# Kernel tuning notes

Measured on AMD Instinct MI355X. Metric: run time of the kernel, lower is better.

Reference implementation:

```python
import jax, jax.numpy as jnp
import numpy as np
import math

B, T, D, H = 4, 1024, 1024, 16
HD = D // H  # 64
ROPE_BASE = 10000.0


def _apply_rope(q, k):
    # q, k: [B, H, T, HD]; interleaved even/odd rotation as in RotaryEmbedding
    t_len = q.shape[2]
    half = q.shape[-1] // 2
    inv_freq = 1.0 / (ROPE_BASE ** (jnp.arange(half, dtype=jnp.float32) / half))
    freqs = jnp.arange(t_len, dtype=jnp.float32)[:, None] * inv_freq  # [T, half]
    cos = jnp.cos(freqs)
    sin = jnp.sin(freqs)

    def rot(u):
        u1 = u[..., ::2]   # even lanes
        u2 = u[..., 1::2]  # odd lanes
        e = u1 * cos - u2 * sin
        o = u2 * cos + u1 * sin
        return jnp.stack([e, o], axis=-1).reshape(u.shape)

    return rot(q), rot(k)


def _split_heads(x):
    b, t, d = x.shape
    return x.reshape(b, t, H, HD).transpose(0, 2, 1, 3)  # [B,H,T,HD]


def _mha(x, Wq, bq, Wk, bk, Wv, bv, Wo, bo, mask):
    q = _split_heads(jnp.einsum('btd,ed->bte', x, Wq) + bq)
    k = _split_heads(jnp.einsum('btd,ed->bte', x, Wk) + bk)
    v = _split_heads(jnp.einsum('btd,ed->bte', x, Wv) + bv)
    q, k = _apply_rope(q, k)
    scores = jnp.einsum('bhtd,bhsd->bhts', q.astype(jnp.float32),
                        k.astype(jnp.float32)) / math.sqrt(HD)
    scores = jnp.where(mask, scores, -jnp.inf)
    attn = jax.nn.softmax(scores, axis=-1).astype(v.dtype)
    ctx = jnp.einsum('bhts,bhsd->bhtd', attn.astype(jnp.float32),
                     v.astype(jnp.float32)).astype(v.dtype)
    ctx = ctx.transpose(0, 2, 1, 3).reshape(x.shape[0], x.shape[1], D)
    z = jnp.einsum('btd,ed->bte', ctx, Wo) + bo
    return z


def setup_inputs() -> dict:
    key = jax.random.key(0)
    ks = jax.random.split(key, 9)
    s = 0.02
    inp = {
        'x':  jax.random.normal(ks[0], (B, T, D), jnp.float32),
        'Wq': jax.random.normal(ks[1], (D, D), jnp.float32) * s,
        'bq': jax.random.normal(ks[2], (D,), jnp.float32) * s,
        'Wk': jax.random.normal(ks[3], (D, D), jnp.float32) * s,
        'bk': jax.random.normal(ks[4], (D,), jnp.float32) * s,
        'Wv': jax.random.normal(ks[5], (D, D), jnp.float32) * s,
        'bv': jax.random.normal(ks[6], (D,), jnp.float32) * s,
        'Wo': jax.random.normal(ks[7], (D, D), jnp.float32) * s,
        'bo': jax.random.normal(ks[8], (D,), jnp.float32) * s,
        'mask': jnp.tril(jnp.ones((T, T), dtype=bool))[None, None],  # causal
    }
    return inp


def reference(x, Wq, bq, Wk, bk, Wv, bv, Wo, bo, mask):
    return _mha(x, Wq, bq, Wk, bk, Wv, bv, Wo, bo, mask)
```

## Files before the change

kernel.cpp:

```cpp
#include <hip/hip_runtime.h>


#define T_SEQ 1024
#define NH    16
#define HDIM  64
#define DM    1024
#define MTOK  4096

typedef __attribute__((ext_vector_type(8))) short short8;
typedef __attribute__((ext_vector_type(4))) float f32x4;
typedef unsigned short u16;

__device__ __forceinline__ u16 f2bf(float f) {
  unsigned int u = __builtin_bit_cast(unsigned int, f);
  u += 0x7fffu + ((u >> 16) & 1u);
  return (u16)(u >> 16);
}

__device__ __forceinline__ void gll16(const void* g, void* l) {
  __builtin_amdgcn_global_load_lds(
      (const __attribute__((address_space(1))) unsigned int*)(unsigned long long)(g),
      (__attribute__((address_space(3))) unsigned int*)(unsigned int)(unsigned long long)(l),
      16, 0, 0);
}

__global__ void prep_kernel(const float* __restrict__ x,
                            const float* __restrict__ Wq, const float* __restrict__ Wk,
                            const float* __restrict__ Wv, const float* __restrict__ Wo,
                            u16* __restrict__ xb, u16* __restrict__ wall,
                            float* __restrict__ ctab, float* __restrict__ stab) {
  const int bid = blockIdx.x, tid = threadIdx.x;
  if (bid < 8192) {
    const float* src;
    u16* dst;
    int i;
    if (bid < 4096) {
      src = x; dst = xb; i = bid * 256 + tid;
    } else {
      const int w = (bid - 4096) >> 10;
      src = w == 0 ? Wq : w == 1 ? Wk : w == 2 ? Wv : Wo;
      dst = wall + (size_t)w * (DM * DM);
      i = ((bid - 4096) & 1023) * 256 + tid;
    }
    float4 f = ((const float4*)src)[i];
    unsigned long long pk = (unsigned long long)f2bf(f.x)
                          | ((unsigned long long)f2bf(f.y) << 16)
                          | ((unsigned long long)f2bf(f.z) << 32)
                          | ((unsigned long long)f2bf(f.w) << 48);
    ((unsigned long long*)dst)[i] = pk;
  } else {
    const int idx = (bid - 8192) * 256 + tid;
    const int t = idx >> 5, i = idx & 31;
    float inv = powf(10000.f, -(float)i * (1.0f / 32.0f));
    float f = (float)t * inv;
    ctab[idx] = cosf(f);
    stab[idx] = sinf(f);
  }
}

template<int BM, int BN, int AI, int BI, int MI, int NJ>
__device__ __forceinline__ void gemm_pipe2(
    const u16* __restrict__ A, const u16* __restrict__ Bw,
    int m0, int n0, u16* As, u16* Bs, f32x4 acc[MI][NJ]) {
  const int tid = threadIdx.x, lane = tid & 63, wave = tid >> 6;
  const int wr = wave >> 1, wc = wave & 1;
  const int srcswz = ((lane & 7) ^ (lane >> 3)) * 8;
  const int NT = DM / 64;

#define STAGE2(t, b)                                                         \
  do {                                                                       \
    _Pragma("unroll") for (int i = 0; i < AI; ++i) {                         \
      const int q = (wave * AI + i) * 64 + lane;                             \
      gll16(&A[(size_t)(m0 + (q >> 3)) * DM + (t) * 64 + srcswz],            \
            &As[(b) * BM * 64 + q * 8]);                                     \
    }                                                                        \
    _Pragma("unroll") for (int i = 0; i < BI; ++i) {                         \
      const int q = (wave * BI + i) * 64 + lane;                             \
      gll16(&Bw[(size_t)(n0 + (q >> 3)) * DM + (t) * 64 + srcswz],           \
            &Bs[(b) * BN * 64 + q * 8]);                                     \
    }                                                                        \
  } while (0)

  STAGE2(0, 0);
  __syncthreads();
  int buf = 0;
  const int arow0 = wr * (BM / 2) + (lane & 15);
  const int brow0 = wc * (BN / 2) + (lane & 15);
  const int c0 = (((lane >> 4)) ^ (lane & 7)) * 8;
  const int c1 = ((4 + (lane >> 4)) ^ (lane & 7)) * 8;
  for (int t = 0; t < NT; ++t) {
    if (t + 1 < NT) STAGE2(t + 1, buf ^ 1);
    short8 af[MI][2], bf[NJ][2];
#pragma unroll
    for (int i = 0; i < MI; ++i) {
      const int r = buf * BM * 64 + (arow0 + i * 16) * 64;
      af[i][0] = *(const short8*)&As[r + c0];
      af[i][1] = *(const short8*)&As[r + c1];
    }
#pragma unroll
    for (int j = 0; j < NJ; ++j) {
      const int r = buf * BN * 64 + (brow0 + j * 16) * 64;
      bf[j][0] = *(const short8*)&Bs[r + c0];
      bf[j][1] = *(const short8*)&Bs[r + c1];
    }
#pragma unroll
    for (int i = 0; i < MI; ++i)
#pragma unroll
      for (int j = 0; j < NJ; ++j) {
        acc[i][j] = __builtin_amdgcn_mfma_f32_16x16x32_bf16(af[i][0], bf[j][0], acc[i][j], 0, 0, 0);
        acc[i][j] = __builtin_amdgcn_mfma_f32_16x16x32_bf16(af[i][1], bf[j][1], acc[i][j], 0, 0, 0);
      }
    __syncthreads();
    buf ^= 1;
  }
#undef STAGE2
}

__global__ __launch_bounds__(256, 2) void qkv_kernel(
    const u16* __restrict__ xb, const u16* __restrict__ wqkv,
    const float* __restrict__ bq, const float* __restrict__ bk, const float* __restrict__ bv,
    const float* __restrict__ ctab, const float* __restrict__ stab,
    u16* __restrict__ qbuf, u16* __restrict__ kbuf, u16* __restrict__ vt) {
  __shared__ __align__(16) u16 As[2 * 128 * 64];
  __shared__ __align__(16) u16 Bs[2 * 192 * 64];
  const int lin = blockIdx.x;
  const int m0 = (lin & 31) * 128;
  const int n0 = (lin >> 5) * 192;
  f32x4 acc[4][6];
#pragma unroll
  for (int i = 0; i < 4; ++i)
#pragma unroll
    for (int j = 0; j < 6; ++j)
#pragma unroll
      for (int r = 0; r < 4; ++r) acc[i][j][r] = 0.f;
  gemm_pipe2<128, 192, 4, 6, 4, 6>(xb, wqkv, m0, n0, As, Bs, acc);

  const int lane = threadIdx.x & 63, wave = threadIdx.x >> 6;
  const int wr = wave >> 1, wc = wave & 1;
#pragma unroll
  for (int i = 0; i < 4; ++i) {
#pragma unroll
    for (int j = 0; j < 6; ++j) {
      const int e = n0 + wc * 96 + j * 16 + (lane & 15);
      const int mode = e >> 10;
      const float* bias = mode == 0 ? bq : (mode == 1 ? bk : bv);
      const float bval = bias[e & 1023];
      const int h = (e >> 6) & 15, hd = e & 63;
#pragma unroll
      for (int r = 0; r < 4; ++r) {
        const int m = m0 + wr * 64 + i * 16 + ((lane >> 4) * 4) + r;
        const int b = m >> 10, t = m & 1023;
        float v = acc[i][j][r] + bval;
        if (mode < 2) {
          float p = __shfl_xor(v, 1);
          const int fi = hd >> 1;
          const float cc = ctab[t * 32 + fi], ss = stab[t * 32 + fi];
          v = (hd & 1) ? (v * cc + p * ss) : (v * cc - p * ss);
          u16* dst = mode == 0 ? qbuf : kbuf;
          dst[(((size_t)(b * NH + h) * T_SEQ + t) << 6) + hd] = f2bf(v);
        } else {
          vt[(((size_t)(b * NH + h) * HDIM + hd) << 10) + t] = f2bf(v);
        }
      }
    }
  }
}

__global__ __launch_bounds__(256) void attn_kernel(
    const u16* __restrict__ qbuf, const u16* __restrict__ kbuf,
    const u16* __restrict__ vtb, u16* __restrict__ ctx) {
  __shared__ __align__(16) u16 Ks[2][64 * 64];
  __shared__ __align__(16) u16 Vs[2][64 * 64];
  __shared__ __align__(16) u16 Psm[4][16 * 64];
  const int bh = blockIdx.x;
  const int b = bh >> 4, h = bh & 15;
  const int tid = threadIdx.x, lane = tid & 63, wave = tid >> 6;
  const u16* Qp = qbuf + (size_t)bh * T_SEQ * HDIM;
  const u16* Kp = kbuf + (size_t)bh * T_SEQ * HDIM;
  const u16* Vp = vtb + (size_t)bh * HDIM * T_SEQ;
  u16* Pw = &Psm[wave][0];
  const float SC = 0.18033688f;

  const int srow = tid >> 3;
  const int schx = ((tid & 7) ^ (srow & 7)) * 8;
  const int lx = lane & 7;

  short8 onesf;
#pragma unroll
  for (int i = 0; i < 8; ++i) onesf[i] = (short)0x3F80;

#define STG(kvt, bb)                                                            \
  do {                                                                          \
    _Pragma("unroll") for (int c = 0; c < 2; ++c) {                             \
      const int rr = c * 32 + srow;                                             \
      gll16(&Kp[(kvt) * 4096 + rr * 64 + schx], &Ks[bb][c * 2048 + tid * 8]);   \
      gll16(&Vp[(size_t)rr * T_SEQ + (kvt) * 64 + schx], &Vs[bb][c * 2048 + tid * 8]); \
    }                                                                           \
  } while (0)

  for (int phase = 0; phase < 2; ++phase) {
    const int qt = phase ? (15 - (int)blockIdx.y) : (int)blockIdx.y;
    const int q0 = qt * 64;
    const int nkv = qt + 1;
    const int qrow = q0 + wave * 16 + (lane & 15);
    const short8 qf0 = *(const short8*)&Qp[qrow * 64 + ((lane >> 4) * 8)];
    const short8 qf1 = *(const short8*)&Qp[qrow * 64 + 32 + ((lane >> 4) * 8)];

    f32x4 acc_o[4], accl;
    float m_r[4];
#pragma unroll
    for (int i = 0; i < 4; ++i) {
#pragma unroll
      for (int r = 0; r < 4; ++r) acc_o[i][r] = 0.f;
      accl[i] = 0.f;
      m_r[i] = -__builtin_inff();
    }

    __syncthreads();
    STG(0, 0);
    int cur = 0;

    for (int kvt = 0; kvt < nkv; ++kvt) {
      __syncthreads();
      if (kvt + 1 < nkv) STG(kvt + 1, cur ^ 1);

      f32x4 sacc[4];
#pragma unroll
      for (int cb = 0; cb < 4; ++cb) {
#pragma unroll
        for (int r = 0; r < 4; ++r) sacc[cb][r] = 0.f;
        const int krow = cb * 16 + (lane & 15);
        const short8 kf0 = *(const short8*)&Ks[cur][krow * 64 + (((lane >> 4) ^ lx) * 8)];
        const short8 kf1 = *(const short8*)&Ks[cur][krow * 64 + (((4 + (lane >> 4)) ^ lx) * 8)];
        sacc[cb] = __builtin_amdgcn_mfma_f32_16x16x32_bf16(qf0, kf0, sacc[cb], 0, 0, 0);
        sacc[cb] = __builtin_amdgcn_mfma_f32_16x16x32_bf16(qf1, kf1, sacc[cb], 0, 0, 0);
      }
      if (kvt == qt) {
        const int trow_base = q0 + wave * 16 + ((lane >> 4) * 4);
#pragma unroll
        for (int cb = 0; cb < 4; ++cb) {
          const int scol = kvt * 64 + cb * 16 + (lane & 15);
#pragma unroll
          for (int r = 0; r < 4; ++r)
            sacc[cb][r] = (scol > trow_base + r) ? -__builtin_inff() : sacc[cb][r] * SC;
        }
      } else {
#pragma unroll
        for (int cb = 0; cb < 4; ++cb)
#pragma unroll
          for (int r = 0; r < 4; ++r) sacc[cb][r] *= SC;
      }
      float mt[4];
#pragma unroll
      for (int r = 0; r < 4; ++r)
        mt[r] = fmaxf(fmaxf(sacc[0][r], sacc[1][r]), fmaxf(sacc[2][r], sacc[3][r]));
#pragma unroll
      for (int off = 1; off < 16; off <<= 1)
#pragma unroll
        for (int r = 0; r < 4; ++r) mt[r] = fmaxf(mt[r], __shfl_xor(mt[r], off));
      float sf[4];
#pragma unroll
      for (int r = 0; r < 4; ++r) {
        const float mn = fmaxf(m_r[r], mt[r]);
        sf[r] = exp2f(m_r[r] - mn);
        m_r[r] = mn;
      }
#pragma unroll
      for (int cb = 0; cb < 4; ++cb)
#pragma unroll
        for (int r = 0; r < 4; ++r) sacc[cb][r] = exp2f(sacc[cb][r] - m_r[r]);
#pragma unroll
      for (int r = 0; r < 4; ++r) accl[r] *= sf[r];
#pragma unroll
      for (int hb = 0; hb < 4; ++hb)
#pragma unroll
        for (int r = 0; r < 4; ++r) acc_o[hb][r] *= sf[r];

#pragma unroll
      for (int cb = 0; cb < 4; ++cb)
#pragma unroll
        for (int r = 0; r < 4; ++r) {
          const int prow = (lane >> 4) * 4 + r;
          Pw[prow * 64 + ((cb * 16 + (lane & 15)) ^ ((prow & 7) << 3))] = f2bf(sacc[cb][r]);
        }

      const int prr = lane & 15;
#pragma unroll
      for (int kc = 0; kc < 2; ++kc) {
        const short8 pf = *(const short8*)&Pw[prr * 64 + (((kc * 4 + (lane >> 4)) ^ lx) * 8)];
        accl = __builtin_amdgcn_mfma_f32_16x16x32_bf16(pf, onesf, accl, 0, 0, 0);
#pragma unroll
        for (int hb = 0; hb < 4; ++hb) {
          const int vrow = hb * 16 + (lane & 15);
          const short8 vf = *(const short8*)&Vs[cur][vrow * 64 + (((kc * 4 + (lane >> 4)) ^ lx) * 8)];
          acc_o[hb] = __builtin_amdgcn_mfma_f32_16x16x32_bf16(pf, vf, acc_o[hb], 0, 0, 0);
        }
      }
      cur ^= 1;
    }

#pragma unroll
    for (int hb = 0; hb < 4; ++hb) {
      const int hd = hb * 16 + (lane & 15);
#pragma unroll
      for (int r = 0; r < 4; ++r) {
        const int t = q0 + wave * 16 + ((lane >> 4) * 4) + r;
        const float v = acc_o[hb][r] / accl[r];
        ctx[((size_t)(b * T_SEQ + t) * NH + h) * HDIM + hd] = f2bf(v);
      }
    }
  }
#undef STG
}

__global__ __launch_bounds__(256, 2) void oproj_kernel(
    const u16* __restrict__ ctx, const u16* __restrict__ Wob,
    const float* __restrict__ bo, float* __restrict__ out) {
  __shared__ __align__(16) u16 As[2 * 64 * 64];
  __shared__ __align__(16) u16 Bs[2 * 128 * 64];
  const int lin = blockIdx.x;
  const int m0 = (lin & 63) * 64;
  const int n0 = (lin >> 6) * 128;
  f32x4 acc[2][4];
#pragma unroll
  for (int i = 0; i < 2; ++i)
#pragma unroll
    for (int j = 0; j < 4; ++j)
#pragma unroll
      for (int r = 0; r < 4; ++r) acc[i][j][r] = 0.f;
  gemm_pipe2<64, 128, 2, 4, 2, 4>(ctx, Wob, m0, n0, As, Bs, acc);
  const int lane = threadIdx.x & 63, wave = threadIdx.x >> 6;
  const int wr = wave >> 1, wc = wave & 1;
#pragma unroll
  for (int i = 0; i < 2; ++i)
#pragma unroll
    for (int j = 0; j < 4; ++j) {
      const int e = n0 + wc * 64 + j * 16 + (lane & 15);
      const float bval = bo[e];
#pragma unroll
      for (int r = 0; r < 4; ++r) {
        const int m = m0 + wr * 32 + i * 16 + ((lane >> 4) * 4) + r;
        out[(size_t)m * DM + e] = acc[i][j][r] + bval;
      }
    }
}

extern "C" void kernel_launch(void* const* d_in, const int* in_sizes, int n_in,
                              void* d_out, int out_size, void* d_ws, size_t ws_size,
                              hipStream_t stream) {
  const float* x  = (const float*)d_in[0];
  const float* Wq = (const float*)d_in[1];
  const float* bq = (const float*)d_in[2];
  const float* Wk = (const float*)d_in[3];
  const float* bk = (const float*)d_in[4];
  const float* Wv = (const float*)d_in[5];
  const float* bv = (const float*)d_in[6];
  const float* Wo = (const float*)d_in[7];
  const float* bo = (const float*)d_in[8];

  char* w = (char*)d_ws;
  u16* xb   = (u16*)(w);
  u16* wall = (u16*)(w + (8ull << 20));
  u16* wob  = (u16*)(w + (14ull << 20));
  u16* qb   = (u16*)(w + (16ull << 20));
  u16* kb   = (u16*)(w + (24ull << 20));
  u16* vtb  = (u16*)(w + (32ull << 20));
  u16* ctxb = (u16*)(w + (40ull << 20));
  float* ctab = (float*)(w + (48ull << 20));
  float* stab = ctab + T_SEQ * 32;

  prep_kernel<<<dim3(8192 + 128), 256, 0, stream>>>(x, Wq, Wk, Wv, Wo, xb, wall, ctab, stab);
  qkv_kernel<<<dim3(512), 256, 0, stream>>>(
      xb, wall, bq, bk, bv, ctab, stab, qb, kb, vtb);
  attn_kernel<<<dim3(64, 8), 256, 0, stream>>>(qb, kb, vtb, ctxb);
  oproj_kernel<<<dim3(512), 256, 0, stream>>>(ctxb, wob, bo, (float*)d_out);
}
```

Measured before the change: 110.6 us.

## Double attention KV tile to 128 and remap QKV GEMM grid to 2D

The attention kernel now processes 128 keys per iteration instead of 64, using dynamic shared memory (80 KB) for double-buffered K/V tiles and wider per-wave P buffers. This halves the loop trip count, cutting per-iteration barriers and softmax reductions, but wastes more masked work on the diagonal tile and may lower occupancy because of the larger LDS footprint. The QKV GEMM launch also moves from a linear grid to a 2D grid, which changes the block ordering and therefore L2 reuse of weight versus activation tiles.

```diff
diff --git a/kernel.cpp b/kernel.cpp
--- a/kernel.cpp
+++ b/kernel.cpp
@@ -123,9 +123,8 @@
     u16* __restrict__ qbuf, u16* __restrict__ kbuf, u16* __restrict__ vt) {
   __shared__ __align__(16) u16 As[2 * 128 * 64];
   __shared__ __align__(16) u16 Bs[2 * 192 * 64];
-  const int lin = blockIdx.x;
-  const int m0 = (lin & 31) * 128;
-  const int n0 = (lin >> 5) * 192;
+  const int m0 = blockIdx.y * 128;
+  const int n0 = blockIdx.x * 192;
   f32x4 acc[4][6];
 #pragma unroll
   for (int i = 0; i < 4; ++i)
@@ -169,42 +168,49 @@
 __global__ __launch_bounds__(256) void attn_kernel(
     const u16* __restrict__ qbuf, const u16* __restrict__ kbuf,
     const u16* __restrict__ vtb, u16* __restrict__ ctx) {
-  __shared__ __align__(16) u16 Ks[2][64 * 64];
-  __shared__ __align__(16) u16 Vs[2][64 * 64];
-  __shared__ __align__(16) u16 Psm[4][16 * 64];
+  extern __shared__ __align__(16) u16 asmem[];
+  u16* Ksm = asmem;
+  u16* Vsm = asmem + 16384;
+  u16* Pall = asmem + 32768;
   const int bh = blockIdx.x;
   const int b = bh >> 4, h = bh & 15;
   const int tid = threadIdx.x, lane = tid & 63, wave = tid >> 6;
   const u16* Qp = qbuf + (size_t)bh * T_SEQ * HDIM;
   const u16* Kp = kbuf + (size_t)bh * T_SEQ * HDIM;
   const u16* Vp = vtb + (size_t)bh * HDIM * T_SEQ;
-  u16* Pw = &Psm[wave][0];
+  u16* Pw = Pall + wave * 2048;
   const float SC = 0.18033688f;
-
-  const int srow = tid >> 3;
-  const int schx = ((tid & 7) ^ (srow & 7)) * 8;
   const int lx = lane & 7;
+  const int q4 = lane >> 4;
 
   short8 onesf;
 #pragma unroll
   for (int i = 0; i < 8; ++i) onesf[i] = (short)0x3F80;
 
-#define STG(kvt, bb)                                                            \
-  do {                                                                          \
-    _Pragma("unroll") for (int c = 0; c < 2; ++c) {                             \
-      const int rr = c * 32 + srow;                                             \
-      gll16(&Kp[(kvt) * 4096 + rr * 64 + schx], &Ks[bb][c * 2048 + tid * 8]);   \
-      gll16(&Vp[(size_t)rr * T_SEQ + (kvt) * 64 + schx], &Vs[bb][c * 2048 + tid * 8]); \
-    }                                                                           \
+#define STG(kvt, bb)                                                             \
+  do {                                                                           \
+    _Pragma("unroll") for (int l = 0; l < 4; ++l) {                              \
+      const int idx = l * 256 + tid;                                             \
+      const int krow = idx >> 3, kch = (idx & 7) ^ (krow & 7);                   \
+      gll16(&Kp[((kvt) * 128 + krow) * 64 + kch * 8], &Ksm[(bb) * 8192 + idx * 8]); \
+    }                                                                            \
+    _Pragma("unroll") for (int l = 0; l < 4; ++l) {                              \
+      const int idx = l * 256 + tid;                                             \
+      const int vrow = idx >> 4, c16 = idx & 15;                                 \
+      const int sc = (c16 & 8) | ((c16 & 7) ^ (vrow & 7));                       \
+      gll16(&Vp[(size_t)vrow * T_SEQ + (kvt) * 128 + sc * 8],                    \
+            &Vsm[(bb) * 8192 + idx * 8]);                                        \
+    }                                                                            \
   } while (0)
 
   for (int phase = 0; phase < 2; ++phase) {
     const int qt = phase ? (15 - (int)blockIdx.y) : (int)blockIdx.y;
     const int q0 = qt * 64;
-    const int nkv = qt + 1;
+    const int dkv = qt >> 1;
+    const int nkv = dkv + 1;
     const int qrow = q0 + wave * 16 + (lane & 15);
-    const short8 qf0 = *(const short8*)&Qp[qrow * 64 + ((lane >> 4) * 8)];
-    const short8 qf1 = *(const short8*)&Qp[qrow * 64 + 32 + ((lane >> 4) * 8)];
+    const short8 qf0 = *(const short8*)&Qp[qrow * 64 + (q4 * 8)];
+    const short8 qf1 = *(const short8*)&Qp[qrow * 64 + 32 + (q4 * 8)];
 
     f32x4 acc_o[4], accl;
     float m_r[4];
@@ -224,36 +230,41 @@
       __syncthreads();
       if (kvt + 1 < nkv) STG(kvt + 1, cur ^ 1);
 
-      f32x4 sacc[4];
-#pragma unroll
-      for (int cb = 0; cb < 4; ++cb) {
+      const u16* Kb = Ksm + cur * 8192;
+      const u16* Vb = Vsm + cur * 8192;
+
+      f32x4 sacc[8];
+#pragma unroll
+      for (int cb = 0; cb < 8; ++cb) {
 #pragma unroll
         for (int r = 0; r < 4; ++r) sacc[cb][r] = 0.f;
         const int krow = cb * 16 + (lane & 15);
-        const short8 kf0 = *(const short8*)&Ks[cur][krow * 64 + (((lane >> 4) ^ lx) * 8)];
-        const short8 kf1 = *(const short8*)&Ks[cur][krow * 64 + (((4 + (lane >> 4)) ^ lx) * 8)];
+        const short8 kf0 = *(const short8*)&Kb[krow * 64 + ((q4 ^ (krow & 7)) * 8)];
+        const short8 kf1 = *(const short8*)&Kb[krow * 64 + (((4 + q4) ^ (krow & 7)) * 8)];
         sacc[cb] = __builtin_amdgcn_mfma_f32_16x16x32_bf16(qf0, kf0, sacc[cb], 0, 0, 0);
         sacc[cb] = __builtin_amdgcn_mfma_f32_16x16x32_bf16(qf1, kf1, sacc[cb], 0, 0, 0);
       }
-      if (kvt == qt) {
-        const int trow_base = q0 + wave * 16 + ((lane >> 4) * 4);
-#pragma unroll
-        for (int cb = 0; cb < 4; ++cb) {
-          const int scol = kvt * 64 + cb * 16 + (lane & 15);
+      if (kvt == dkv) {
+        const int trow_base = q0 + wave * 16 + q4 * 4;
+#pragma unroll
+        for (int cb = 0; cb < 8; ++cb) {
+          const int scol = kvt * 128 + cb * 16 + (lane & 15);
 #pragma unroll
           for (int r = 0; r < 4; ++r)
             sacc[cb][r] = (scol > trow_base + r) ? -__builtin_inff() : sacc[cb][r] * SC;
         }
       } else {
 #pragma unroll
-        for (int cb = 0; cb < 4; ++cb)
+        for (int cb = 0; cb < 8; ++cb)
 #pragma unroll
           for (int r = 0; r < 4; ++r) sacc[cb][r] *= SC;
       }
       float mt[4];
 #pragma unroll
-      for (int r = 0; r < 4; ++r)
+      for (int r = 0; r < 4; ++r) {
         mt[r] = fmaxf(fmaxf(sacc[0][r], sacc[1][r]), fmaxf(sacc[2][r], sacc[3][r]));
+        mt[r] = fmaxf(mt[r], fmaxf(fmaxf(sacc[4][r], sacc[5][r]), fmaxf(sacc[6][r], sacc[7][r])));
+      }
 #pragma unroll
       for (int off = 1; off < 16; off <<= 1)
 #pragma unroll
@@ -266,7 +277,7 @@
         m_r[r] = mn;
       }
 #pragma unroll
-      for (int cb = 0; cb < 4; ++cb)
+      for (int cb = 0; cb < 8; ++cb)
 #pragma unroll
         for (int r = 0; r < 4; ++r) sacc[cb][r] = exp2f(sacc[cb][r] - m_r[r]);
 #pragma unroll
@@ -277,22 +288,26 @@
         for (int r = 0; r < 4; ++r) acc_o[hb][r] *= sf[r];
 
 #pragma unroll
-      for (int cb = 0; cb < 4; ++cb)
+      for (int cb = 0; cb < 8; ++cb)
 #pragma unroll
         for (int r = 0; r < 4; ++r) {
-          const int prow = (lane >> 4) * 4 + r;
-          Pw[prow * 64 + ((cb * 16 + (lane & 15)) ^ ((prow & 7) << 3))] = f2bf(sacc[cb][r]);
+          const int prow = q4 * 4 + r;
+          const int col = cb * 16 + (lane & 15);
+          Pw[prow * 128 + (col & 64) + ((col & 63) ^ ((prow & 7) << 3))] = f2bf(sacc[cb][r]);
         }
 
       const int prr = lane & 15;
 #pragma unroll
-      for (int kc = 0; kc < 2; ++kc) {
-        const short8 pf = *(const short8*)&Pw[prr * 64 + (((kc * 4 + (lane >> 4)) ^ lx) * 8)];
+      for (int kc = 0; kc < 4; ++kc) {
+        const int lc = kc * 4 + q4;
+        const int pc = (lc & 8) | ((lc & 7) ^ (prr & 7));
+        const short8 pf = *(const short8*)&Pw[prr * 128 + pc * 8];
         accl = __builtin_amdgcn_mfma_f32_16x16x32_bf16(pf, onesf, accl, 0, 0, 0);
 #pragma unroll
         for (int hb = 0; hb < 4; ++hb) {
           const int vrow = hb * 16 + (lane & 15);
-          const short8 vf = *(const short8*)&Vs[cur][vrow * 64 + (((kc * 4 + (lane >> 4)) ^ lx) * 8)];
+          const int vc = (lc & 8) | ((lc & 7) ^ (vrow & 7));
+          const short8 vf = *(const short8*)&Vb[vrow * 128 + vc * 8];
           acc_o[hb] = __builtin_amdgcn_mfma_f32_16x16x32_bf16(pf, vf, acc_o[hb], 0, 0, 0);
         }
       }
@@ -304,7 +319,7 @@
       const int hd = hb * 16 + (lane & 15);
 #pragma unroll
       for (int r = 0; r < 4; ++r) {
-        const int t = q0 + wave * 16 + ((lane >> 4) * 4) + r;
+        const int t = q0 + wave * 16 + q4 * 4 + r;
         const float v = acc_o[hb][r] / accl[r];
         ctx[((size_t)(b * T_SEQ + t) * NH + h) * HDIM + hd] = f2bf(v);
       }
@@ -369,9 +384,12 @@
   float* ctab = (float*)(w + (48ull << 20));
   float* stab = ctab + T_SEQ * 32;
 
+  hipFuncSetAttribute(reinterpret_cast<const void*>(attn_kernel),
+                      hipFuncAttributeMaxDynamicSharedMemorySize, 81920);
+
   prep_kernel<<<dim3(8192 + 128), 256, 0, stream>>>(x, Wq, Wk, Wv, Wo, xb, wall, ctab, stab);
-  qkv_kernel<<<dim3(512), 256, 0, stream>>>(
+  qkv_kernel<<<dim3(3 * DM / 192, MTOK / 128), 256, 0, stream>>>(
       xb, wall, bq, bk, bv, ctab, stab, qb, kb, vtb);
-  attn_kernel<<<dim3(64, 8), 256, 0, stream>>>(qb, kb, vtb, ctxb);
+  attn_kernel<<<dim3(64, 8), 256, 81920, stream>>>(qb, kb, vtb, ctxb);
   oproj_kernel<<<dim3(512), 256, 0, stream>>>(ctxb, wob, bo, (float*)d_out);
 }
```

Result: faster. 105.8 us (-4.4%).
